# Optimization experiments

Hardware: AMD Instinct MI355X
Metric: run time of the kernel (lower is better)

The kernel has to match this reference:

```python
import jax, jax.numpy as jnp
import numpy as np

N_HEADS = 8
D_HEAD = 64
SCALE = 1.0 / np.sqrt(D_HEAD)  # ProbAttention default scale = 1/sqrt(D)


def setup_inputs() -> dict:
    key = jax.random.key(0)
    ks = jax.random.split(key, 8)
    B, L_dec, L_enc, D = 4, 2048, 2048, 512
    factor = 5
    sample_k = int(factor * np.ceil(np.log(L_enc)))  # 40
    n_top = int(factor * np.ceil(np.log(L_dec)))     # 40
    w = lambda k: jax.random.normal(k, (D, D), jnp.float32) * (1.0 / np.sqrt(D))
    return {
        "x": jax.random.normal(ks[0], (B, L_dec, D), jnp.float32),
        "context": jax.random.normal(ks[1], (B, L_enc, D), jnp.float32),
        "Wq": w(ks[2]), "bq": jnp.zeros((D,), jnp.float32),
        "Wk": w(ks[3]), "bk": jnp.zeros((D,), jnp.float32),
        "Wv": w(ks[4]), "bv": jnp.zeros((D,), jnp.float32),
        "Wo": w(ks[5]), "bo": jnp.zeros((D,), jnp.float32),
        "index_sample": jax.random.randint(ks[6], (L_dec, sample_k), 0, L_enc, jnp.int32),
        "n_top": n_top,
    }


def reference(x, context, Wq, bq, Wk, bk, Wv, bv, Wo, bo, index_sample, n_top):
    B, L_dec, D = x.shape
    L_enc = context.shape[1]
    H, Dh = N_HEADS, D_HEAD
    # QKV projections (torch Linear: y = x @ W.T + b), then [B,H,L,Dh]
    Q = (x @ Wq.T + bq).reshape(B, L_dec, H, Dh).transpose(0, 2, 1, 3)
    K = (context @ Wk.T + bk).reshape(B, L_enc, H, Dh).transpose(0, 2, 1, 3)
    V = (context @ Wv.T + bv).reshape(B, L_enc, H, Dh).transpose(0, 2, 1, 3)
    # --- _prob_QK: sample keys per query, measure sparsity, pick top queries ---
    K_sample = K[:, :, index_sample, :]                    # [B,H,L_dec,sample_k,Dh]
    QK_sample = jnp.einsum('bhld,bhlsd->bhls', Q, K_sample)
    M = QK_sample.max(-1) - QK_sample.sum(-1) / L_enc      # [B,H,L_dec]
    _, top_idx = jax.lax.top_k(M, n_top)                   # [B,H,u]
    Q_red = jnp.take_along_axis(Q, top_idx[..., None], axis=2)  # [B,H,u,Dh]
    scores = jnp.einsum('bhud,bhkd->bhuk', Q_red, K) * SCALE
    # --- initial context: mean of V (mask_flag=False) ---
    ctx = jnp.broadcast_to(V.mean(axis=2, keepdims=True), (B, H, L_dec, Dh))
    # --- update selected query positions with full attention ---
    attn = jax.nn.softmax(scores, axis=-1)
    upd = jnp.einsum('bhuk,bhkd->bhud', attn, V)           # [B,H,u,Dh]
    b_idx = jnp.arange(B)[:, None, None]
    h_idx = jnp.arange(H)[None, :, None]
    ctx = ctx.at[b_idx, h_idx, top_idx].set(upd)
    out = ctx.transpose(0, 2, 1, 3).reshape(B, L_dec, D)
    return out @ Wo.T + bo                                  # dropout = identity (eval)
```

## Files before the change

### kernel.cpp

```cpp
#include <hip/hip_runtime.h>
#include <float.h>

#define BATCH 4
#define LSEQ  2048
#define DMODEL 512
#define NH    8
#define DHD   64
#define NSAMP 40
#define NTOP  40
#define NSEG  16
#define SEGK  128
#define SUBK  64
#define QK_SCALE 0.125f

typedef unsigned short u16;
typedef __attribute__((ext_vector_type(8))) short short8b;
typedef __attribute__((ext_vector_type(4))) float f32x4;
typedef __attribute__((ext_vector_type(4))) float f32x4v;

#define ASTRIDE ((size_t)BATCH * LSEQ * DMODEL)
#define WSTRIDE ((size_t)DMODEL * DMODEL)

static __device__ __forceinline__ u16 f2bf(float x) {
    unsigned u = __float_as_uint(x);
    u += 0x7FFFu + ((u >> 16) & 1u);
    return (u16)(u >> 16);
}
static __device__ __forceinline__ float bf2f(u16 s) {
    return __uint_as_float((unsigned)s << 16);
}
static __device__ __forceinline__ void split2(
    const float4 v, ushort4& o1, ushort4& o2)
{
    const float in[4] = {v.x, v.y, v.z, v.w};
    u16 a[4], b[4];
#pragma unroll
    for (int c = 0; c < 4; ++c) {
        a[c] = f2bf(in[c]);
        b[c] = f2bf(in[c] - bf2f(a[c]));
    }
    o1.x = a[0]; o1.y = a[1]; o1.z = a[2]; o1.w = a[3];
    o2.x = b[0]; o2.y = b[1]; o2.z = b[2]; o2.w = b[3];
}

__global__ __launch_bounds__(256) void split3_all(
    const float* __restrict__ x, const float* __restrict__ ctxin,
    const float* __restrict__ Wq, const float* __restrict__ Wk,
    const float* __restrict__ Wv,
    u16* __restrict__ xsP, u16* __restrict__ csP,
    u16* __restrict__ wqP, u16* __restrict__ wkP, u16* __restrict__ wvP,
    float* __restrict__ VmeanRaw, float* __restrict__ uacc,
    float* __restrict__ wsum)
{
    const int flat = blockIdx.x;
    if (flat < 8)         VmeanRaw[flat * 256 + threadIdx.x] = 0.f;
    else if (flat < 328)  uacc[(flat - 8) * 256 + threadIdx.x] = 0.f;
    else if (flat < 333) { const int j = (flat - 328) * 256 + threadIdx.x;
                           if (j < BATCH * NH * NTOP) wsum[j] = 0.f; }

    const int X4 = 1 << 20;
    const int W4 = 1 << 16;
    const int total = 2 * X4 + 3 * W4;
    for (int i = blockIdx.x * 256 + threadIdx.x; i < total; i += gridDim.x * 256) {
        const float* src; u16* dst; size_t pstride; int i4;
        if (i < X4)            { src = x;     dst = xsP; pstride = ASTRIDE; i4 = i; }
        else if (i < 2 * X4)   { src = ctxin; dst = csP; pstride = ASTRIDE; i4 = i - X4; }
        else {
            const int w = i - 2 * X4;
            const int which = w >> 16, rem = w & (W4 - 1);
            src = (which == 0) ? Wq : (which == 1) ? Wk : Wv;
            dst = (which == 0) ? wqP : (which == 1) ? wkP : wvP;
            pstride = WSTRIDE; i4 = rem;
        }
        const float4 v = reinterpret_cast<const float4*>(src)[i4];
        const float in[4] = {v.x, v.y, v.z, v.w};
        ushort4 o1, o2, o3;
        u16 b1[4], b2[4], b3[4];
#pragma unroll
        for (int c = 0; c < 4; ++c) {
            const float xx = in[c];
            b1[c] = f2bf(xx);
            const float r1 = xx - bf2f(b1[c]);
            b2[c] = f2bf(r1);
            b3[c] = f2bf(r1 - bf2f(b2[c]));
        }
        o1.x = b1[0]; o1.y = b1[1]; o1.z = b1[2]; o1.w = b1[3];
        o2.x = b2[0]; o2.y = b2[1]; o2.z = b2[2]; o2.w = b2[3];
        o3.x = b3[0]; o3.y = b3[1]; o3.z = b3[2]; o3.w = b3[3];
        reinterpret_cast<ushort4*>(dst)[i4]                = o1;
        reinterpret_cast<ushort4*>(dst + pstride)[i4]      = o2;
        reinterpret_cast<ushort4*>(dst + 2 * pstride)[i4]  = o3;
    }
}

__global__ __launch_bounds__(256) void gemm_all(
    const u16* __restrict__ xsP, const u16* __restrict__ csP,
    const u16* __restrict__ wqP, const u16* __restrict__ wkP,
    const u16* __restrict__ wvP,
    const float* __restrict__ bq, const float* __restrict__ bk,
    const float* __restrict__ bv,
    float* __restrict__ Qt, float* __restrict__ Kt, float* __restrict__ Vt,
    float* __restrict__ VmeanRaw)
{
    const int z = blockIdx.y;
    const int i = blockIdx.x;
    const int xcd = i & 7;
    const int loc = i >> 3;
    const int m0 = (xcd * 8 + (loc & 7)) * 128;
    const int n0 = (loc >> 3) * 128;

    const u16* __restrict__ Ap   = (z == 0) ? xsP : csP;
    const u16* __restrict__ Wp   = (z == 0) ? wqP : (z == 1 ? wkP : wvP);
    const float* __restrict__ bias = (z == 0) ? bq : (z == 1 ? bk : bv);
    float*       __restrict__ Out  = (z == 0) ? Qt : (z == 1 ? Kt : Vt);
    const int npl = (z == 2) ? 2 : 3;

    __shared__ u16 As[3][128][40];
    __shared__ u16 Ws[3][128][40];

    const int tid  = threadIdx.x;
    const int w    = tid >> 6;
    const int lane = tid & 63;
    const int wm   = w >> 1;
    const int wn   = w & 1;
    const int lr   = lane & 15;
    const int lg   = lane >> 4;

    const int srow = tid >> 1;
    const int sc   = (tid & 1) * 16;

    f32x4 acc[4][4];
#pragma unroll
    for (int mf = 0; mf < 4; ++mf)
#pragma unroll
        for (int nf = 0; nf < 4; ++nf)
#pragma unroll
            for (int r = 0; r < 4; ++r) acc[mf][nf][r] = 0.f;

    short8b sa[3][2], sw[3][2];
#pragma unroll
    for (int p = 0; p < 3; ++p) {
        if (p < npl) {
            const u16* asrc = Ap + p * ASTRIDE + (size_t)(m0 + srow) * DMODEL + sc;
            const u16* wsrc = Wp + p * WSTRIDE + (size_t)(n0 + srow) * DMODEL + sc;
            sa[p][0] = *reinterpret_cast<const short8b*>(asrc);
            sa[p][1] = *reinterpret_cast<const short8b*>(asrc + 8);
            sw[p][0] = *reinterpret_cast<const short8b*>(wsrc);
            sw[p][1] = *reinterpret_cast<const short8b*>(wsrc + 8);
        }
    }

    for (int k0 = 0; k0 < DMODEL; k0 += 32) {
#pragma unroll
        for (int p = 0; p < 3; ++p) {
            if (p < npl) {
                *reinterpret_cast<short8b*>(&As[p][srow][sc])     = sa[p][0];
                *reinterpret_cast<short8b*>(&As[p][srow][sc + 8]) = sa[p][1];
                *reinterpret_cast<short8b*>(&Ws[p][srow][sc])     = sw[p][0];
                *reinterpret_cast<short8b*>(&Ws[p][srow][sc + 8]) = sw[p][1];
            }
        }
        __syncthreads();

        if (k0 + 32 < DMODEL) {
#pragma unroll
            for (int p = 0; p < 3; ++p) {
                if (p < npl) {
                    const u16* asrc =
                        Ap + p * ASTRIDE + (size_t)(m0 + srow) * DMODEL + k0 + 32 + sc;
                    const u16* wsrc =
                        Wp + p * WSTRIDE + (size_t)(n0 + srow) * DMODEL + k0 + 32 + sc;
                    sa[p][0] = *reinterpret_cast<const short8b*>(asrc);
                    sa[p][1] = *reinterpret_cast<const short8b*>(asrc + 8);
                    sw[p][0] = *reinterpret_cast<const short8b*>(wsrc);
                    sw[p][1] = *reinterpret_cast<const short8b*>(wsrc + 8);
                }
            }
        }

        short8b af[4][3];
#pragma unroll
        for (int mf = 0; mf < 4; ++mf) {
            const int row = wm * 64 + mf * 16 + lr;
#pragma unroll
            for (int p = 0; p < 3; ++p)
                if (p < npl)
                    af[mf][p] = *reinterpret_cast<const short8b*>(&As[p][row][lg * 8]);
        }
#pragma unroll
        for (int nf = 0; nf < 4; ++nf) {
            const int row = wn * 64 + nf * 16 + lr;
            const short8b b1 = *reinterpret_cast<const short8b*>(&Ws[0][row][lg * 8]);
            const short8b b2 = *reinterpret_cast<const short8b*>(&Ws[1][row][lg * 8]);
#pragma unroll
            for (int mf = 0; mf < 4; ++mf) {
                acc[mf][nf] = __builtin_amdgcn_mfma_f32_16x16x32_bf16(af[mf][0], b1, acc[mf][nf], 0, 0, 0);
                acc[mf][nf] = __builtin_amdgcn_mfma_f32_16x16x32_bf16(af[mf][1], b1, acc[mf][nf], 0, 0, 0);
                acc[mf][nf] = __builtin_amdgcn_mfma_f32_16x16x32_bf16(af[mf][0], b2, acc[mf][nf], 0, 0, 0);
            }
            if (z != 2) {
                const short8b b3 = *reinterpret_cast<const short8b*>(&Ws[2][row][lg * 8]);
#pragma unroll
                for (int mf = 0; mf < 4; ++mf) {
                    acc[mf][nf] = __builtin_amdgcn_mfma_f32_16x16x32_bf16(af[mf][2], b1, acc[mf][nf], 0, 0, 0);
                    acc[mf][nf] = __builtin_amdgcn_mfma_f32_16x16x32_bf16(af[mf][0], b3, acc[mf][nf], 0, 0, 0);
                    acc[mf][nf] = __builtin_amdgcn_mfma_f32_16x16x32_bf16(af[mf][1], b2, acc[mf][nf], 0, 0, 0);
                }
            }
        }
        __syncthreads();
    }

#pragma unroll
    for (int nf = 0; nf < 4; ++nf) {
        const int n = n0 + wn * 64 + nf * 16 + lr;
        const int h = n >> 6, d = n & 63;
        const float bv_ = bias[n];
        float cs = 0.f;
#pragma unroll
        for (int mf = 0; mf < 4; ++mf) {
#pragma unroll
            for (int r = 0; r < 4; ++r) {
                const int m = m0 + wm * 64 + mf * 16 + lg * 4 + r;
                const int b = m >> 11, l = m & (LSEQ - 1);
                const float val = acc[mf][nf][r] + bv_;
                Out[((size_t)(b * NH + h) * LSEQ + l) * DHD + d] = val;
                cs += val;
            }
        }
        if (z == 2)
            atomicAdd(&VmeanRaw[((m0 >> 11) * NH + h) * DHD + d], cs);
    }
}

__global__ __launch_bounds__(256) void score_kernel(
    const float* __restrict__ Qt, const float* __restrict__ Kt,
    const int* __restrict__ idxs, float* __restrict__ M)
{
    const int flat = blockIdx.x;
    const int xcd  = flat & 7;
    const int slot = flat >> 3;
    const int bh   = xcd * 4 + (slot >> 9);
    const int w    = threadIdx.x >> 6;
    const int lane = threadIdx.x & 63;
    const int l    = (slot & 511) * 4 + w;

    const int g  = lane >> 4;
    const int dl = lane & 15;

#if defined(__has_builtin) && __has_builtin(__builtin_nontemporal_load)
    const f32x4v q4 = __builtin_nontemporal_load(
        reinterpret_cast<const f32x4v*>(Qt + ((size_t)bh * LSEQ + l) * DHD + dl * 4));
#else
    const f32x4v q4 = *reinterpret_cast<const f32x4v*>(
        Qt + ((size_t)bh * LSEQ + l) * DHD + dl * 4);
#endif

    const float* Kb = Kt + (size_t)bh * LSEQ * DHD;
    float vmax = -FLT_MAX, vsum = 0.f;
#pragma unroll
    for (int it = 0; it < 10; ++it) {
        const int s = it * 4 + g;
        const int ks = idxs[l * NSAMP + s];
        const float4 k4 = *reinterpret_cast<const float4*>(
            Kb + (size_t)ks * DHD + dl * 4);
        float p = q4[0] * k4.x + q4[1] * k4.y + q4[2] * k4.z + q4[3] * k4.w;
        p += __shfl_xor(p, 1);
        p += __shfl_xor(p, 2);
        p += __shfl_xor(p, 4);
        p += __shfl_xor(p, 8);
        vmax = fmaxf(vmax, p);
        vsum += p;
    }
    vmax = fmaxf(vmax, __shfl_xor(vmax, 16));
    vsum += __shfl_xor(vsum, 16);
    vmax = fmaxf(vmax, __shfl_xor(vmax, 32));
    vsum += __shfl_xor(vsum, 32);
    if (lane == 0) M[(size_t)bh * LSEQ + l] = vmax - vsum * (1.0f / LSEQ);
}

__global__ __launch_bounds__(256) void topk_kernel(
    const float* __restrict__ M, int* __restrict__ topidx,
    const float* __restrict__ VmeanRaw, const float* __restrict__ Wo,
    const float* __restrict__ bo, float* __restrict__ meanout)
{
    const int bh = blockIdx.x;

    if (bh >= 32) {
        const int b = bh - 32;
        __shared__ float mc[DMODEL];
        for (int i = threadIdx.x; i < DMODEL; i += 256)
            mc[i] = VmeanRaw[b * DMODEL + i] * (1.0f / (float)LSEQ);
        __syncthreads();
        for (int n = threadIdx.x; n < DMODEL; n += 256) {
            float acc = bo[n];
            const float* wr = Wo + (size_t)n * DMODEL;
            for (int k = 0; k < DMODEL; ++k) acc = fmaf(mc[k], wr[k], acc);
            meanout[b * DMODEL + n] = acc;
        }
        return;
    }

    const int w = threadIdx.x >> 6, lane = threadIdx.x & 63;
    const int base = threadIdx.x * 8;

    float e[8];
    {
        const float4 v0 = *reinterpret_cast<const float4*>(M + (size_t)bh * LSEQ + base);
        const float4 v1 = *reinterpret_cast<const float4*>(M + (size_t)bh * LSEQ + base + 4);
        e[0] = v0.x; e[1] = v0.y; e[2] = v0.z; e[3] = v0.w;
        e[4] = v1.x; e[5] = v1.y; e[6] = v1.z; e[7] = v1.w;
    }

    __shared__ float rv[4];
    __shared__ int   ri[4];
    __shared__ int   winner;

    for (int t = 0; t < NTOP; ++t) {
        float bv = e[0]; int br = 0;
#pragma unroll
        for (int r = 1; r < 8; ++r)
            if (e[r] > bv) { bv = e[r]; br = r; }
        int bi = base + br;
#pragma unroll
        for (int off = 32; off; off >>= 1) {
            const float ov = __shfl_xor(bv, off);
            const int   oi = __shfl_xor(bi, off);
            if (ov > bv || (ov == bv && oi < bi)) { bv = ov; bi = oi; }
        }
        if (lane == 0) { rv[w] = bv; ri[w] = bi; }
        __syncthreads();
        if (threadIdx.x == 0) {
            float fv = rv[0]; int fi = ri[0];
#pragma unroll
            for (int k = 1; k < 4; ++k)
                if (rv[k] > fv || (rv[k] == fv && ri[k] < fi)) { fv = rv[k]; fi = ri[k]; }
            topidx[bh * NTOP + t] = fi;
            winner = fi;
        }
        __syncthreads();
        const int fi = winner;
        if ((fi >> 3) == threadIdx.x) e[fi & 7] = -FLT_MAX;
    }
}

__global__ __launch_bounds__(256) void attn_partial(
    const float* __restrict__ Qt, const float* __restrict__ Kt,
    const float* __restrict__ Vt, const int* __restrict__ topidx,
    float* __restrict__ wsum, float* __restrict__ uacc)
{
    const int bh  = blockIdx.x;
    const int seg = blockIdx.y;
    const int tid = threadIdx.x;
    const int w    = tid >> 6;
    const int lane = tid & 63;
    const int lr = lane & 15, lg = lane >> 4;

    __shared__ u16 Qs[2][48][72];
    __shared__ u16 Ks[2][64][72];
    __shared__ u16 Vtl[2][64][72];
    __shared__ float wsl[48];

    for (int i = tid; i < 48 * 16; i += 256) {
        const int row = i >> 4, c = i & 15;
        float4 v = make_float4(0.f, 0.f, 0.f, 0.f);
        if (row < NTOP) {
            const int l = topidx[bh * NTOP + row];
            v = *reinterpret_cast<const float4*>(
                Qt + ((size_t)bh * LSEQ + l) * DHD + c * 4);
        }
        ushort4 o1, o2;
        split2(v, o1, o2);
        *reinterpret_cast<ushort4*>(&Qs[0][row][c * 4]) = o1;
        *reinterpret_cast<ushort4*>(&Qs[1][row][c * 4]) = o2;
    }
    if (tid < 48) wsl[tid] = 0.f;

    f32x4 pvacc[3];
#pragma unroll
    for (int qt = 0; qt < 3; ++qt)
#pragma unroll
        for (int r = 0; r < 4; ++r) pvacc[qt][r] = 0.f;

    for (int sub = 0; sub < 2; ++sub) {
        const int kbase = seg * SEGK + sub * SUBK;
        __syncthreads();

        for (int i = tid; i < 64 * 16; i += 256) {
            const int key = i >> 4, c = i & 15;
            const size_t g = ((size_t)bh * LSEQ + kbase + key) * DHD + c * 4;
            const float4 kv = *reinterpret_cast<const float4*>(Kt + g);
            const float4 vv = *reinterpret_cast<const float4*>(Vt + g);
            ushort4 k1, k2, v1, v2;
            split2(kv, k1, k2);
            split2(vv, v1, v2);
            *reinterpret_cast<ushort4*>(&Ks[0][key][c * 4]) = k1;
            *reinterpret_cast<ushort4*>(&Ks[1][key][c * 4]) = k2;
            Vtl[0][c * 4 + 0][key] = v1.x; Vtl[0][c * 4 + 1][key] = v1.y;
            Vtl[0][c * 4 + 2][key] = v1.z; Vtl[0][c * 4 + 3][key] = v1.w;
            Vtl[1][c * 4 + 0][key] = v2.x; Vtl[1][c * 4 + 1][key] = v2.y;
            Vtl[1][c * 4 + 2][key] = v2.z; Vtl[1][c * 4 + 3][key] = v2.w;
        }
        __syncthreads();

        f32x4 acc[3];
#pragma unroll
        for (int qt = 0; qt < 3; ++qt)
#pragma unroll
            for (int r = 0; r < 4; ++r) acc[qt][r] = 0.f;
#pragma unroll
        for (int ks = 0; ks < 2; ++ks) {
            const short8b b1 = *reinterpret_cast<const short8b*>(
                &Ks[0][w * 16 + lr][ks * 32 + lg * 8]);
            const short8b b2 = *reinterpret_cast<const short8b*>(
                &Ks[1][w * 16 + lr][ks * 32 + lg * 8]);
#pragma unroll
            for (int qt = 0; qt < 3; ++qt) {
                const short8b a1 = *reinterpret_cast<const short8b*>(
                    &Qs[0][qt * 16 + lr][ks * 32 + lg * 8]);
                const short8b a2 = *reinterpret_cast<const short8b*>(
                    &Qs[1][qt * 16 + lr][ks * 32 + lg * 8]);
                acc[qt] = __builtin_amdgcn_mfma_f32_16x16x32_bf16(a1, b1, acc[qt], 0, 0, 0);
                acc[qt] = __builtin_amdgcn_mfma_f32_16x16x32_bf16(a2, b1, acc[qt], 0, 0, 0);
                acc[qt] = __builtin_amdgcn_mfma_f32_16x16x32_bf16(a1, b2, acc[qt], 0, 0, 0);
            }
        }
        __syncthreads();

#pragma unroll
        for (int qt = 0; qt < 3; ++qt) {
#pragma unroll
            for (int r = 0; r < 4; ++r) {
                const float e = __expf(acc[qt][r] * QK_SCALE);
                float s = e;
                s += __shfl_xor(s, 1);
                s += __shfl_xor(s, 2);
                s += __shfl_xor(s, 4);
                s += __shfl_xor(s, 8);
                const int q = qt * 16 + lg * 4 + r;
                if (lr == 0) atomicAdd(&wsl[q], s);
                const u16 p1 = f2bf(e);
                const u16 p2 = f2bf(e - bf2f(p1));
                Ks[0][q][w * 16 + lr] = p1;
                Ks[1][q][w * 16 + lr] = p2;
            }
        }
        __syncthreads();

#pragma unroll
        for (int ks = 0; ks < 2; ++ks) {
            const short8b b1 = *reinterpret_cast<const short8b*>(
                &Vtl[0][w * 16 + lr][ks * 32 + lg * 8]);
            const short8b b2 = *reinterpret_cast<const short8b*>(
                &Vtl[1][w * 16 + lr][ks * 32 + lg * 8]);
#pragma unroll
            for (int qt = 0; qt < 3; ++qt) {
                const short8b a1 = *reinterpret_cast<const short8b*>(
                    &Ks[0][qt * 16 + lr][ks * 32 + lg * 8]);
                const short8b a2 = *reinterpret_cast<const short8b*>(
                    &Ks[1][qt * 16 + lr][ks * 32 + lg * 8]);
                pvacc[qt] = __builtin_amdgcn_mfma_f32_16x16x32_bf16(a1, b1, pvacc[qt], 0, 0, 0);
                pvacc[qt] = __builtin_amdgcn_mfma_f32_16x16x32_bf16(a2, b1, pvacc[qt], 0, 0, 0);
                pvacc[qt] = __builtin_amdgcn_mfma_f32_16x16x32_bf16(a1, b2, pvacc[qt], 0, 0, 0);
            }
        }
    }

#pragma unroll
    for (int qt = 0; qt < 3; ++qt) {
#pragma unroll
        for (int r = 0; r < 4; ++r) {
            const int q = qt * 16 + lg * 4 + r;
            if (q < NTOP)
                atomicAdd(&uacc[((size_t)bh * NTOP + q) * DHD + w * 16 + lr],
                          pvacc[qt][r]);
        }
    }
    if (tid < NTOP) atomicAdd(&wsum[bh * NTOP + tid], wsl[tid]);
}

__global__ __launch_bounds__(256) void finalize_base(
    const float* __restrict__ wsum, const float* __restrict__ uacc,
    const float* __restrict__ VmeanRaw, const float* __restrict__ meanout,
    float* __restrict__ delta, float* __restrict__ out)
{
    const int blk = blockIdx.x;
    if (blk < 320) {
        const int idx = blk * 256 + threadIdx.x;
        const int bh = idx / 2560;
        const int rem = idx - bh * 2560;
        const int q = rem >> 6, d = rem & 63;
        const float vm = VmeanRaw[bh * DHD + d] * (1.0f / (float)LSEQ);
        delta[idx] = uacc[idx] / wsum[bh * NTOP + q] - vm;
    } else {
        const int total4 = BATCH * LSEQ * (DMODEL / 4);
        for (int i = (blk - 320) * 256 + threadIdx.x; i < total4; i += 2048 * 256) {
            const int row = i >> 7;
            const int b = row >> 11;
            const int c = i & 127;
            reinterpret_cast<float4*>(out)[i] =
                reinterpret_cast<const float4*>(meanout)[b * 128 + c];
        }
    }
}

__global__ __launch_bounds__(128) void out_scatter(
    const int* __restrict__ topidx, const float* __restrict__ delta,
    const float* __restrict__ Wo, float* __restrict__ out)
{
    const int bh = blockIdx.x;
    const int u  = blockIdx.y;
    const int b = bh >> 3, h = bh & 7;
    const int l = topidx[bh * NTOP + u];

    __shared__ float dl[DHD];
    if (threadIdx.x < DHD)
        dl[threadIdx.x] = delta[((size_t)bh * NTOP + u) * DHD + threadIdx.x];
    __syncthreads();

    float* orow = out + ((size_t)b * LSEQ + l) * DMODEL;
#pragma unroll
    for (int c = 0; c < 4; ++c) {
        const int n = threadIdx.x * 4 + c;
        const float4* wr4 = reinterpret_cast<const float4*>(
            Wo + (size_t)n * DMODEL + h * DHD);
        float a = 0.f;
#pragma unroll
        for (int dd = 0; dd < 16; ++dd) {
            const float4 wv = wr4[dd];
            a += dl[dd * 4 + 0] * wv.x + dl[dd * 4 + 1] * wv.y +
                 dl[dd * 4 + 2] * wv.z + dl[dd * 4 + 3] * wv.w;
        }
        atomicAdd(&orow[n], a);
    }
}

extern "C" void kernel_launch(void* const* d_in, const int* in_sizes, int n_in,
                              void* d_out, int out_size, void* d_ws, size_t ws_size,
                              hipStream_t stream)
{
    (void)in_sizes; (void)n_in; (void)out_size; (void)ws_size;
    const float* x     = (const float*)d_in[0];
    const float* ctxin = (const float*)d_in[1];
    const float* Wq    = (const float*)d_in[2];
    const float* bq    = (const float*)d_in[3];
    const float* Wk    = (const float*)d_in[4];
    const float* bk    = (const float*)d_in[5];
    const float* Wv    = (const float*)d_in[6];
    const float* bv    = (const float*)d_in[7];
    const float* Wo    = (const float*)d_in[8];
    const float* bo    = (const float*)d_in[9];
    const int*   idxs  = (const int*)d_in[10];
    float* out = (float*)d_out;

    char* ws = (char*)d_ws;
    size_t off = 0;
    auto alloc = [&](size_t bytes) -> void* {
        void* p = ws + off;
        off += (bytes + 255) & ~(size_t)255;
        return p;
    };

    const size_t qkv_bytes = (size_t)BATCH * NH * LSEQ * DHD * sizeof(float);
    float*         Qt       = (float*)alloc(qkv_bytes);
    float*         Kt       = (float*)alloc(qkv_bytes);
    float*         Vt       = (float*)alloc(qkv_bytes);
    float*         Mbuf     = (float*)alloc((size_t)BATCH * NH * LSEQ * sizeof(float));
    float*         VmeanRaw = (float*)alloc((size_t)BATCH * NH * DHD * sizeof(float));
    float*         meanout  = (float*)alloc((size_t)BATCH * DMODEL * sizeof(float));
    float*         delta    = (float*)alloc((size_t)BATCH * NH * NTOP * DHD * sizeof(float));
    int*           topidx   = (int*)alloc((size_t)BATCH * NH * NTOP * sizeof(int));
    float*         wsum     = (float*)alloc((size_t)BATCH * NH * NTOP * sizeof(float));
    float*         uacc     = (float*)alloc((size_t)BATCH * NH * NTOP * DHD * sizeof(float));
    u16*           xsP      = (u16*)alloc(ASTRIDE * 3 * 2);
    u16*           csP      = (u16*)alloc(ASTRIDE * 3 * 2);
    u16*           wqP      = (u16*)alloc(WSTRIDE * 3 * 2);
    u16*           wkP      = (u16*)alloc(WSTRIDE * 3 * 2);
    u16*           wvP      = (u16*)alloc(WSTRIDE * 3 * 2);

    split3_all<<<2048, 256, 0, stream>>>(x, ctxin, Wq, Wk, Wv,
                                         xsP, csP, wqP, wkP, wvP,
                                         VmeanRaw, uacc, wsum);

    gemm_all<<<dim3(256, 3), 256, 0, stream>>>(
        xsP, csP, wqP, wkP, wvP, bq, bk, bv, Qt, Kt, Vt, VmeanRaw);

    score_kernel<<<(BATCH * NH * LSEQ) / 4, 256, 0, stream>>>(
        Qt, Kt, idxs, Mbuf);

    topk_kernel<<<36, 256, 0, stream>>>(
        Mbuf, topidx, VmeanRaw, Wo, bo, meanout);

    attn_partial<<<dim3(BATCH * NH, NSEG), 256, 0, stream>>>(
        Qt, Kt, Vt, topidx, wsum, uacc);

    finalize_base<<<2368, 256, 0, stream>>>(
        wsum, uacc, VmeanRaw, meanout, delta, out);

    out_scatter<<<dim3(BATCH * NH, NTOP), 128, 0, stream>>>(
        topidx, delta, Wo, out);
}
```

Before: 224.6 us.

## Fuse finalize into attention and scatter kernels; flatten GEMM grid for XCD mapping

```diff
diff --git a/kernel.cpp b/kernel.cpp
--- a/kernel.cpp
+++ b/kernel.cpp
@@ -102,10 +102,11 @@
     float* __restrict__ Qt, float* __restrict__ Kt, float* __restrict__ Vt,
     float* __restrict__ VmeanRaw)
 {
-    const int z = blockIdx.y;
     const int i = blockIdx.x;
     const int xcd = i & 7;
-    const int loc = i >> 3;
+    const int rest = i >> 3;
+    const int z   = rest % 3;
+    const int loc = rest / 3;
     const int m0 = (xcd * 8 + (loc & 7)) * 128;
     const int n0 = (loc >> 3) * 128;
 
@@ -347,7 +348,8 @@
 __global__ __launch_bounds__(256) void attn_partial(
     const float* __restrict__ Qt, const float* __restrict__ Kt,
     const float* __restrict__ Vt, const int* __restrict__ topidx,
-    float* __restrict__ wsum, float* __restrict__ uacc)
+    float* __restrict__ wsum, float* __restrict__ uacc,
+    const float* __restrict__ meanout, float* __restrict__ out)
 {
     const int bh  = blockIdx.x;
     const int seg = blockIdx.y;
@@ -477,24 +479,11 @@
         }
     }
     if (tid < NTOP) atomicAdd(&wsum[bh * NTOP + tid], wsl[tid]);
-}
-
-__global__ __launch_bounds__(256) void finalize_base(
-    const float* __restrict__ wsum, const float* __restrict__ uacc,
-    const float* __restrict__ VmeanRaw, const float* __restrict__ meanout,
-    float* __restrict__ delta, float* __restrict__ out)
-{
-    const int blk = blockIdx.x;
-    if (blk < 320) {
-        const int idx = blk * 256 + threadIdx.x;
-        const int bh = idx / 2560;
-        const int rem = idx - bh * 2560;
-        const int q = rem >> 6, d = rem & 63;
-        const float vm = VmeanRaw[bh * DHD + d] * (1.0f / (float)LSEQ);
-        delta[idx] = uacc[idx] / wsum[bh * NTOP + q] - vm;
-    } else {
-        const int total4 = BATCH * LSEQ * (DMODEL / 4);
-        for (int i = (blk - 320) * 256 + threadIdx.x; i < total4; i += 2048 * 256) {
+
+    {
+        const int blkid = bh * NSEG + seg;
+        const int base4 = blkid * 2048;
+        for (int i = base4 + tid; i < base4 + 2048; i += 256) {
             const int row = i >> 7;
             const int b = row >> 11;
             const int c = i & 127;
@@ -505,7 +494,8 @@
 }
 
 __global__ __launch_bounds__(128) void out_scatter(
-    const int* __restrict__ topidx, const float* __restrict__ delta,
+    const int* __restrict__ topidx, const float* __restrict__ wsum,
+    const float* __restrict__ uacc, const float* __restrict__ VmeanRaw,
     const float* __restrict__ Wo, float* __restrict__ out)
 {
     const int bh = blockIdx.x;
@@ -514,8 +504,12 @@
     const int l = topidx[bh * NTOP + u];
 
     __shared__ float dl[DHD];
-    if (threadIdx.x < DHD)
-        dl[threadIdx.x] = delta[((size_t)bh * NTOP + u) * DHD + threadIdx.x];
+    if (threadIdx.x < DHD) {
+        const float inv = 1.0f / wsum[bh * NTOP + u];
+        const float vm = VmeanRaw[bh * DHD + threadIdx.x] * (1.0f / (float)LSEQ);
+        dl[threadIdx.x] =
+            uacc[((size_t)bh * NTOP + u) * DHD + threadIdx.x] * inv - vm;
+    }
     __syncthreads();
 
     float* orow = out + ((size_t)b * LSEQ + l) * DMODEL;
@@ -568,7 +562,6 @@
     float*         Mbuf     = (float*)alloc((size_t)BATCH * NH * LSEQ * sizeof(float));
     float*         VmeanRaw = (float*)alloc((size_t)BATCH * NH * DHD * sizeof(float));
     float*         meanout  = (float*)alloc((size_t)BATCH * DMODEL * sizeof(float));
-    float*         delta    = (float*)alloc((size_t)BATCH * NH * NTOP * DHD * sizeof(float));
     int*           topidx   = (int*)alloc((size_t)BATCH * NH * NTOP * sizeof(int));
     float*         wsum     = (float*)alloc((size_t)BATCH * NH * NTOP * sizeof(float));
     float*         uacc     = (float*)alloc((size_t)BATCH * NH * NTOP * DHD * sizeof(float));
@@ -582,7 +575,7 @@
                                          xsP, csP, wqP, wkP, wvP,
                                          VmeanRaw, uacc, wsum);
 
-    gemm_all<<<dim3(256, 3), 256, 0, stream>>>(
+    gemm_all<<<768, 256, 0, stream>>>(
         xsP, csP, wqP, wkP, wvP, bq, bk, bv, Qt, Kt, Vt, VmeanRaw);
 
     score_kernel<<<(BATCH * NH * LSEQ) / 4, 256, 0, stream>>>(
@@ -592,11 +585,8 @@
         Mbuf, topidx, VmeanRaw, Wo, bo, meanout);
 
     attn_partial<<<dim3(BATCH * NH, NSEG), 256, 0, stream>>>(
-        Qt, Kt, Vt, topidx, wsum, uacc);
-
-    finalize_base<<<2368, 256, 0, stream>>>(
-        wsum, uacc, VmeanRaw, meanout, delta, out);
+        Qt, Kt, Vt, topidx, wsum, uacc, meanout, out);
 
     out_scatter<<<dim3(BATCH * NH, NTOP), 128, 0, stream>>>(
-        topidx, delta, Wo, out);
-}
+        topidx, wsum, uacc, VmeanRaw, Wo, out);
+}
```

Result: slower. 237.7 us (+5.8%).
